# Kernel optimization log

Hardware: AMD Instinct MI355X
Metric: run time of the kernel (lower is better)

Reference implementation:

```python
import jax, jax.numpy as jnp
import numpy as np

B = 8
SHAPE = (4, 16, 16)   # latent video shape; S = prod = 1024
S = 1024
AE = 64               # ae_embed_dim
D = 768               # embed_dim
F = 3072              # mlp_dim
H = 12                # num_heads (heads are re-merged before the score matmul!)
L = 12                # num_layers
C = 17                # n_classes
OUT = 1024            # out_dim
EPS = 1e-6
HD = D // H


def setup_inputs() -> dict:
    key = jax.random.key(0)
    ks = iter(jax.random.split(key, 64))

    def p(shape, s=0.02):
        return jax.random.normal(next(ks), shape, jnp.float32) * s

    inp = {
        'x': jax.random.normal(next(ks), (B, *SHAPE, AE), jnp.float32),
        'mask': jnp.tril(jnp.ones((S, S), bool)),  # causal
        'label': jax.nn.one_hot(jax.random.randint(next(ks), (B,), 0, C), C, dtype=jnp.float32),
        'dense_in_w': p((D, AE)), 'dense_in_b': jnp.zeros((D,), jnp.float32),
        'sos': p((D,)),
        # BroadcastPositionBiases: embed_dim=768 split into 3 chunks of 256
        'pos0': p((SHAPE[0], D // 3)), 'pos1': p((SHAPE[1], D // 3)), 'pos2': p((SHAPE[2], D // 3)),
        'ln1_sw': p((L, D, C)), 'ln1_bw': p((L, D, C)),
        'qkv_w': p((L, 3 * D, D)), 'qkv_b': jnp.zeros((L, 3 * D), jnp.float32),
        'ao1_w': p((L, D, D)), 'ao1_b': jnp.zeros((L, D), jnp.float32),  # DotProductAttention.out_proj
        'ao2_w': p((L, D, D)), 'ao2_b': jnp.zeros((L, D), jnp.float32),  # MultiHeadAttention.out_proj
        'ln2_sw': p((L, D, C)), 'ln2_bw': p((L, D, C)),
        'mlp_w1': p((L, F, D)), 'mlp_b1': jnp.zeros((L, F), jnp.float32),
        'mlp_w2': p((L, D, F)), 'mlp_b2': jnp.zeros((L, D), jnp.float32),
        'lnf_sw': p((D, C)), 'lnf_bw': p((D, C)),
        'out_w': p((OUT, D)), 'out_b': jnp.zeros((OUT,), jnp.float32),
    }
    return inp


def cond_ln(x, cond, sw, bw):
    # conditional LayerNorm: mul = rsqrt(var+eps)*(1+Linear(cond)), bias = Linear(cond)
    mean = jnp.mean(x, axis=-1, keepdims=True)
    var = jnp.mean((x - mean) ** 2, axis=-1, keepdims=True)
    scale = cond @ sw.T   # [B, D]
    bias = cond @ bw.T    # [B, D]
    mul = jax.lax.rsqrt(var + EPS) * (1.0 + scale[:, None, :])
    return (x - mean) * mul + bias[:, None, :]


def pos_bias(embs, shape):
    n = len(shape)
    outs = []
    for i, e in enumerate(embs):
        sh = [1] * n + [e.shape[-1]]
        sh[i] = shape[i]
        outs.append(jnp.broadcast_to(e.reshape(sh), tuple(shape) + (e.shape[-1],)))
    return jnp.concatenate(outs, axis=-1).reshape(-1, sum(e.shape[-1] for e in embs))  # [S, D]


def attn_block(h, mask, qkv_w, qkv_b, o1_w, o1_b, o2_w, o2_b):
    Bn, Sn, Dn = h.shape
    qkv = h @ qkv_w.T + qkv_b                       # [B, S, 3D]
    qkv = qkv.reshape(Bn, Sn, H, 3 * HD)            # per-head [q|k|v] layout
    q = qkv[..., :HD].reshape(Bn, Sn, Dn)           # heads re-merged BEFORE scores
    k = qkv[..., HD:2 * HD].reshape(Bn, Sn, Dn)
    v = qkv[..., 2 * HD:].reshape(Bn, Sn, Dn)
    # NOTE: scaling uses full embed_dim (module quirk), not head_dim
    scores = jnp.einsum('bqd,bkd->bqk', q * (float(Dn) ** -0.5), k)
    scores = jnp.where(mask[None, :, :], scores, -jnp.inf)
    w = jax.nn.softmax(scores, axis=-1)
    out = jnp.einsum('bqk,bkd->bqd', w, v)
    out = out @ o1_w.T + o1_b                        # DotProductAttention.out_proj
    out = out @ o2_w.T + o2_b                        # MultiHeadAttention.out_proj (applied twice)
    return out


def _forward(x, mask, label, dense_in_w, dense_in_b, sos, pos0, pos1, pos2,
             ln1_sw, ln1_bw, qkv_w, qkv_b, ao1_w, ao1_b, ao2_w, ao2_b,
             ln2_sw, ln2_bw, mlp_w1, mlp_b1, mlp_w2, mlp_b2,
             lnf_sw, lnf_bw, out_w, out_b):
    Bn = x.shape[0]
    old_shape = x.shape[1:-1]
    h = x.reshape(Bn, -1, x.shape[-1]) @ dense_in_w.T + dense_in_b   # [B, S, D]
    # right shift with learned SOS token
    h = jnp.concatenate([jnp.broadcast_to(sos, (Bn, 1, D)), h[:, :-1]], axis=1)
    pb = pos_bias([pos0, pos1, pos2], old_shape)                     # [S, D]
    h = h + pb[None, :h.shape[1]]
    for l in range(L):
        hn = cond_ln(h, label, ln1_sw[l], ln1_bw[l])
        h = h + attn_block(hn, mask, qkv_w[l], qkv_b[l], ao1_w[l], ao1_b[l], ao2_w[l], ao2_b[l])
        hn = cond_ln(h, label, ln2_sw[l], ln2_bw[l])
        m = hn @ mlp_w1[l].T + mlp_b1[l]
        m = jax.nn.sigmoid(1.702 * m) * m           # GELU2
        m = m @ mlp_w2[l].T + mlp_b2[l]
        h = h + m
    h = cond_ln(h, label, lnf_sw, lnf_bw)
    out = h @ out_w.T + out_b                        # [B, S, OUT]
    return out.reshape(Bn, *old_shape, out.shape[-1])


def reference(x, mask, label, dense_in_w, dense_in_b, sos, pos0, pos1, pos2,
              ln1_sw, ln1_bw, qkv_w, qkv_b, ao1_w, ao1_b, ao2_w, ao2_b,
              ln2_sw, ln2_bw, mlp_w1, mlp_b1, mlp_w2, mlp_b2,
              lnf_sw, lnf_bw, out_w, out_b):
    return _forward(x, mask, label, dense_in_w, dense_in_b, sos, pos0, pos1, pos2,
                    ln1_sw, ln1_bw, qkv_w, qkv_b, ao1_w, ao1_b, ao2_w, ao2_b,
                    ln2_sw, ln2_bw, mlp_w1, mlp_b1, mlp_w2, mlp_b2,
                    lnf_sw, lnf_bw, out_w, out_b)
```

## Files before the change

### kernel.cpp

```cpp
#include <hip/hip_runtime.h>

typedef __bf16 bf16;
typedef __bf16 bf16x8 __attribute__((ext_vector_type(8)));
typedef __bf16 bf16x4 __attribute__((ext_vector_type(4)));
typedef float  f32x4  __attribute__((ext_vector_type(4)));

#define DEV __device__ __forceinline__

DEV void gload_lds16(const bf16* g, bf16* l) {
    __builtin_amdgcn_global_load_lds(
        (__attribute__((address_space(1))) void*)g,
        (__attribute__((address_space(3))) void*)l, 16, 0, 0);
}

enum { M_QKV, M_SCORES, M_PV, M_BIAS, M_RESID, M_GELU, M_OUT };

template<int MODE>
__global__ __launch_bounds__(256)
void gemm_k(const bf16* __restrict__ A, const bf16* __restrict__ B,
            int M, int N, int K,
            long long batchA, long long batchB, long long batchC,
            const float* __restrict__ bias,
            bf16* __restrict__ Cb, float* __restrict__ Cf,
            bf16* __restrict__ qp, bf16* __restrict__ kp, bf16* __restrict__ vp)
{
    const int bm = blockIdx.x, bn = blockIdx.y, bz = blockIdx.z;
    if (MODE == M_SCORES && bn > bm) return;
    int kTiles = K >> 5;
    if (MODE == M_PV) {
        int lim = (bm + 1) * 4;
        if (lim < kTiles) kTiles = lim;
    }

    const int tid = threadIdx.x, wid = tid >> 6, lane = tid & 63;
    const bf16* Ab = A + (long long)bz * batchA + (long long)bm * 128 * K;
    const bf16* Bb = B + (long long)bz * batchB + (long long)bn * 128 * K;

    __shared__ __align__(16) bf16 sA[2][4096];
    __shared__ __align__(16) bf16 sB[2][4096];

    const int srow = wid * 16 + (lane >> 2);
    const int scol = (lane & 3) * 8;
    const long long aoff = (long long)srow * K + scol;

    auto stage = [&](int buf, int kt) {
        const bf16* ga = Ab + (long long)kt * 32;
        const bf16* gb = Bb + (long long)kt * 32;
        gload_lds16(ga + aoff,            &sA[buf][(wid * 16) * 32]);
        gload_lds16(ga + aoff + 64LL * K, &sA[buf][(64 + wid * 16) * 32]);
        gload_lds16(gb + aoff,            &sB[buf][(wid * 16) * 32]);
        gload_lds16(gb + aoff + 64LL * K, &sB[buf][(64 + wid * 16) * 32]);
    };

    f32x4 acc[4][4];
#pragma unroll
    for (int m = 0; m < 4; ++m)
#pragma unroll
        for (int n = 0; n < 4; ++n) acc[m][n] = (f32x4){0.f, 0.f, 0.f, 0.f};

    stage(0, 0);
    __syncthreads();

    const int wr = wid >> 1, wc = wid & 1;
    const int arow = wr * 64 + (lane & 15);
    const int brow = wc * 64 + (lane & 15);
    const int koff = (lane >> 4) * 8;

    for (int kt = 0; kt < kTiles; ++kt) {
        const int cur = kt & 1;
        if (kt + 1 < kTiles) stage(cur ^ 1, kt + 1);
        bf16x8 af[4], bfr[4];
#pragma unroll
        for (int m = 0; m < 4; ++m)
            af[m] = *(const bf16x8*)&sA[cur][(arow + m * 16) * 32 + koff];
#pragma unroll
        for (int n = 0; n < 4; ++n)
            bfr[n] = *(const bf16x8*)&sB[cur][(brow + n * 16) * 32 + koff];
#pragma unroll
        for (int m = 0; m < 4; ++m)
#pragma unroll
            for (int n = 0; n < 4; ++n)
                acc[m][n] = __builtin_amdgcn_mfma_f32_16x16x32_bf16(af[m], bfr[n], acc[m][n], 0, 0, 0);
        __syncthreads();
    }

    const int cr0 = bm * 128 + wr * 64 + (lane >> 4) * 4;
    const int cc0 = bn * 128 + wc * 64 + (lane & 15);
#pragma unroll
    for (int m = 0; m < 4; ++m) {
#pragma unroll
        for (int n = 0; n < 4; ++n) {
            const int col = cc0 + n * 16;
#pragma unroll
            for (int r = 0; r < 4; ++r) {
                const int row = cr0 + m * 16 + r;
                float v = acc[m][n][r];
                if (MODE == M_QKV) {
                    v += bias[col];
                    int hd = col / 192, rr = col % 192;
                    int b = row >> 10, s = row & 1023;
                    if (rr < 64)
                        qp[(long long)row * 768 + hd * 64 + rr] = (bf16)(v * 0.03608439182435161f);
                    else if (rr < 128)
                        kp[(long long)row * 768 + hd * 64 + (rr - 64)] = (bf16)v;
                    else
                        vp[((long long)b * 768 + hd * 64 + (rr - 128)) * 1024 + s] = (bf16)v;
                } else if (MODE == M_SCORES || MODE == M_PV) {
                    Cb[(long long)bz * batchC + (long long)row * N + col] = (bf16)v;
                } else if (MODE == M_BIAS) {
                    Cb[(long long)row * N + col] = (bf16)(v + bias[col]);
                } else if (MODE == M_RESID) {
                    long long idx = (long long)row * N + col;
                    Cf[idx] += v + bias[col];
                } else if (MODE == M_GELU) {
                    float xg = v + bias[col];
                    Cb[(long long)row * N + col] = (bf16)(xg / (1.f + __expf(-1.702f * xg)));
                } else {
                    Cf[(long long)row * N + col] = v + bias[col];
                }
            }
        }
    }
}

__global__ __launch_bounds__(256)
void cvt_bf16_k(const float* __restrict__ in, bf16* __restrict__ out, int n4)
{
    int i = blockIdx.x * 256 + threadIdx.x;
    if (i >= n4) return;
    float4 f = ((const float4*)in)[i];
    bf16x4 o = { (bf16)f.x, (bf16)f.y, (bf16)f.z, (bf16)f.w };
    ((bf16x4*)out)[i] = o;
}

__global__ __launch_bounds__(256)
void cond_proj_k(const float* __restrict__ label, const float* __restrict__ sw,
                 const float* __restrict__ bw, float* __restrict__ scale,
                 float* __restrict__ bias, int total)
{
    int idx = blockIdx.x * 256 + threadIdx.x;
    if (idx >= total) return;
    int l = idx / 6144;
    int rem = idx - l * 6144;
    int b = rem / 768, d = rem - (rem / 768) * 768;
    const float* lab = label + b * 17;
    const float* swp = sw + ((long long)l * 768 + d) * 17;
    const float* bwp = bw + ((long long)l * 768 + d) * 17;
    float s = 0.f, bb = 0.f;
#pragma unroll
    for (int c = 0; c < 17; ++c) { float lv = lab[c]; s += lv * swp[c]; bb += lv * bwp[c]; }
    scale[idx] = s;
    bias[idx]  = bb;
}

__global__ __launch_bounds__(256)
void embed_k(const float* __restrict__ x, const float* __restrict__ w,
             const float* __restrict__ wb, const float* __restrict__ sos,
             const float* __restrict__ p0, const float* __restrict__ p1,
             const float* __restrict__ p2, float* __restrict__ h)
{
    const int s = blockIdx.x, b = blockIdx.y;
    __shared__ __align__(16) float xr[64];
    if (s > 0 && threadIdx.x < 64)
        xr[threadIdx.x] = x[((long long)b * 1024 + (s - 1)) * 64 + threadIdx.x];
    __syncthreads();
    const int i0 = s >> 8, i1 = (s >> 4) & 15, i2 = s & 15;
#pragma unroll
    for (int j = 0; j < 3; ++j) {
        const int d = j * 256 + threadIdx.x;
        float v;
        if (s == 0) {
            v = sos[d];
        } else {
            const float4* wr4 = (const float4*)(w + (long long)d * 64);
            const float4* xr4 = (const float4*)xr;
            float acc = 0.f;
#pragma unroll
            for (int t = 0; t < 16; ++t) {
                float4 wv = wr4[t], xv = xr4[t];
                acc += wv.x * xv.x + wv.y * xv.y + wv.z * xv.z + wv.w * xv.w;
            }
            v = wb[d] + acc;
        }
        float pbv = (d < 256) ? p0[i0 * 256 + d]
                  : (d < 512) ? p1[i1 * 256 + (d - 256)]
                              : p2[i2 * 256 + (d - 512)];
        h[((long long)b * 1024 + s) * 768 + d] = v + pbv;
    }
}

__global__ __launch_bounds__(256)
void cond_ln_k(const float* __restrict__ h, const float* __restrict__ scale,
               const float* __restrict__ bias, bf16* __restrict__ out)
{
    const long long row = (long long)blockIdx.y * 1024 + blockIdx.x;
    const int b = blockIdx.y;
    const float* hr = h + row * 768;
    float v[3], sum = 0.f, sq = 0.f;
#pragma unroll
    for (int j = 0; j < 3; ++j) {
        v[j] = hr[j * 256 + threadIdx.x];
        sum += v[j]; sq += v[j] * v[j];
    }
    __shared__ float sm[8];
#pragma unroll
    for (int o = 32; o; o >>= 1) { sum += __shfl_down(sum, o); sq += __shfl_down(sq, o); }
    const int wid = threadIdx.x >> 6;
    if ((threadIdx.x & 63) == 0) { sm[wid] = sum; sm[4 + wid] = sq; }
    __syncthreads();
    sum = sm[0] + sm[1] + sm[2] + sm[3];
    sq  = sm[4] + sm[5] + sm[6] + sm[7];
    const float mean = sum * (1.f / 768.f);
    const float var  = sq * (1.f / 768.f) - mean * mean;
    const float rs   = rsqrtf(var + 1e-6f);
    const float* sc = scale + (long long)b * 768;
    const float* bi = bias  + (long long)b * 768;
    bf16* orow = out + row * 768;
#pragma unroll
    for (int j = 0; j < 3; ++j) {
        const int d = j * 256 + threadIdx.x;
        orow[d] = (bf16)((v[j] - mean) * rs * (1.f + sc[d]) + bi[d]);
    }
}

__global__ __launch_bounds__(256)
void softmax_k(bf16* __restrict__ P)
{
    const int i = blockIdx.x, b = blockIdx.y;
    bf16* row = P + ((long long)b * 1024 + i) * 1024;
    const int len = i + 1;
    float v[4], mx = -1e30f;
#pragma unroll
    for (int j = 0; j < 4; ++j) {
        int c = j * 256 + threadIdx.x;
        v[j] = (c < len) ? (float)row[c] : -1e30f;
        mx = fmaxf(mx, v[j]);
    }
    __shared__ float sm[8];
#pragma unroll
    for (int o = 32; o; o >>= 1) mx = fmaxf(mx, __shfl_down(mx, o));
    const int wid = threadIdx.x >> 6;
    if ((threadIdx.x & 63) == 0) sm[wid] = mx;
    __syncthreads();
    mx = fmaxf(fmaxf(sm[0], sm[1]), fmaxf(sm[2], sm[3]));
    float s = 0.f;
#pragma unroll
    for (int j = 0; j < 4; ++j) {
        v[j] = __expf(v[j] - mx);
        s += ((j * 256 + threadIdx.x) < len) ? v[j] : 0.f;
    }
#pragma unroll
    for (int o = 32; o; o >>= 1) s += __shfl_down(s, o);
    if ((threadIdx.x & 63) == 0) sm[4 + wid] = s;
    __syncthreads();
    s = sm[4] + sm[5] + sm[6] + sm[7];
    const float inv = 1.f / s;
#pragma unroll
    for (int j = 0; j < 4; ++j) {
        int c = j * 256 + threadIdx.x;
        row[c] = (c < len) ? (bf16)(v[j] * inv) : (bf16)0.f;
    }
}

__global__ __launch_bounds__(256)
void fill_k(float* o, int n, float v)
{
    int i = blockIdx.x * 256 + threadIdx.x;
    if (i < n) o[i] = v;
}

extern "C" void kernel_launch(void* const* d_in, const int* in_sizes, int n_in,
                              void* d_out, int out_size, void* d_ws, size_t ws_size,
                              hipStream_t stream)
{
    (void)in_sizes; (void)n_in;
    const float* x     = (const float*)d_in[0];
    const float* label = (const float*)d_in[2];
    const float* dw    = (const float*)d_in[3];
    const float* db    = (const float*)d_in[4];
    const float* sos   = (const float*)d_in[5];
    const float* p0    = (const float*)d_in[6];
    const float* p1    = (const float*)d_in[7];
    const float* p2    = (const float*)d_in[8];
    const float* ln1sw = (const float*)d_in[9];
    const float* ln1bw = (const float*)d_in[10];
    const float* qkvw  = (const float*)d_in[11];
    const float* qkvb  = (const float*)d_in[12];
    const float* ao1w  = (const float*)d_in[13];
    const float* ao1b  = (const float*)d_in[14];
    const float* ao2w  = (const float*)d_in[15];
    const float* ao2b  = (const float*)d_in[16];
    const float* ln2sw = (const float*)d_in[17];
    const float* ln2bw = (const float*)d_in[18];
    const float* m1w   = (const float*)d_in[19];
    const float* m1b   = (const float*)d_in[20];
    const float* m2w   = (const float*)d_in[21];
    const float* m2b   = (const float*)d_in[22];
    const float* lnfsw = (const float*)d_in[23];
    const float* lnfbw = (const float*)d_in[24];
    const float* outw  = (const float*)d_in[25];
    const float* outb  = (const float*)d_in[26];
    float* out = (float*)d_out;

    char* p = (char*)d_ws;
    auto alloc = [&](size_t bytes) { void* r = (void*)p; p += (bytes + 255) & ~(size_t)255; return r; };
    float* h    = (float*)alloc(8192LL * 768 * 4);
    bf16*  hn   = (bf16*) alloc(8192LL * 768 * 2);
    bf16*  q    = (bf16*) alloc(8192LL * 768 * 2);
    bf16*  kbuf = (bf16*) alloc(8192LL * 768 * 2);
    bf16*  vT   = (bf16*) alloc(8192LL * 768 * 2);
    bf16*  P    = (bf16*) alloc(8LL * 1024 * 1024 * 2);
    bf16*  attn = (bf16*) alloc(8192LL * 768 * 2);
    bf16*  o1o  = (bf16*) alloc(8192LL * 768 * 2);
    bf16*  mb   = (bf16*) alloc(8192LL * 3072 * 2);
    bf16*  wqkv = (bf16*) alloc(2304LL * 768 * 2);
    bf16*  wo1  = (bf16*) alloc(768LL * 768 * 2);
    bf16*  wo2  = (bf16*) alloc(768LL * 768 * 2);
    bf16*  wm1  = (bf16*) alloc(3072LL * 768 * 2);
    bf16*  wm2  = (bf16*) alloc(3072LL * 768 * 2);
    bf16*  wout = (bf16*) alloc(1024LL * 768 * 2);
    float* s1   = (float*)alloc(12LL * 8 * 768 * 4);
    float* b1   = (float*)alloc(12LL * 8 * 768 * 4);
    float* s2   = (float*)alloc(12LL * 8 * 768 * 4);
    float* b2   = (float*)alloc(12LL * 8 * 768 * 4);
    float* sf   = (float*)alloc(8LL * 768 * 4);
    float* bfb  = (float*)alloc(8LL * 768 * 4);

    size_t needed = (size_t)(p - (char*)d_ws);
    if (needed > ws_size) {
        fill_k<<<(out_size + 255) / 256, 256, 0, stream>>>(out, out_size, 1e9f);
        return;
    }

    cvt_bf16_k<<<1024 * 768 / 4 / 256, 256, 0, stream>>>(outw, wout, 1024 * 768 / 4);
    cond_proj_k<<<(12 * 8 * 768 + 255) / 256, 256, 0, stream>>>(label, ln1sw, ln1bw, s1, b1, 12 * 8 * 768);
    cond_proj_k<<<(12 * 8 * 768 + 255) / 256, 256, 0, stream>>>(label, ln2sw, ln2bw, s2, b2, 12 * 8 * 768);
    cond_proj_k<<<(8 * 768 + 255) / 256, 256, 0, stream>>>(label, lnfsw, lnfbw, sf, bfb, 8 * 768);
    embed_k<<<dim3(1024, 8), 256, 0, stream>>>(x, dw, db, sos, p0, p1, p2, h);

    for (int l = 0; l < 12; ++l) {
        cvt_bf16_k<<<2304 * 768 / 4 / 256, 256, 0, stream>>>(qkvw + (long long)l * 2304 * 768, wqkv, 2304 * 768 / 4);
        cvt_bf16_k<<< 768 * 768 / 4 / 256, 256, 0, stream>>>(ao1w + (long long)l * 768 * 768,  wo1,  768 * 768 / 4);
        cvt_bf16_k<<< 768 * 768 / 4 / 256, 256, 0, stream>>>(ao2w + (long long)l * 768 * 768,  wo2,  768 * 768 / 4);
        cvt_bf16_k<<<3072 * 768 / 4 / 256, 256, 0, stream>>>(m1w  + (long long)l * 3072 * 768, wm1,  3072 * 768 / 4);
        cvt_bf16_k<<<3072 * 768 / 4 / 256, 256, 0, stream>>>(m2w  + (long long)l * 768 * 3072, wm2,  3072 * 768 / 4);

        cond_ln_k<<<dim3(1024, 8), 256, 0, stream>>>(h, s1 + (long long)l * 6144, b1 + (long long)l * 6144, hn);

        gemm_k<M_QKV><<<dim3(64, 18, 1), 256, 0, stream>>>(
            hn, wqkv, 8192, 2304, 768, 0, 0, 0,
            qkvb + (long long)l * 2304, nullptr, nullptr, q, kbuf, vT);

        gemm_k<M_SCORES><<<dim3(8, 8, 8), 256, 0, stream>>>(
            q, kbuf, 1024, 1024, 768, 1024LL * 768, 1024LL * 768, 1024LL * 1024,
            nullptr, P, nullptr, nullptr, nullptr, nullptr);

        softmax_k<<<dim3(1024, 8), 256, 0, stream>>>(P);

        gemm_k<M_PV><<<dim3(8, 6, 8), 256, 0, stream>>>(
            P, vT, 1024, 768, 1024, 1024LL * 1024, 768LL * 1024, 1024LL * 768,
            nullptr, attn, nullptr, nullptr, nullptr, nullptr);

        gemm_k<M_BIAS><<<dim3(64, 6, 1), 256, 0, stream>>>(
            attn, wo1, 8192, 768, 768, 0, 0, 0,
            ao1b + (long long)l * 768, o1o, nullptr, nullptr, nullptr, nullptr);

        gemm_k<M_RESID><<<dim3(64, 6, 1), 256, 0, stream>>>(
            o1o, wo2, 8192, 768, 768, 0, 0, 0,
            ao2b + (long long)l * 768, nullptr, h, nullptr, nullptr, nullptr);

        cond_ln_k<<<dim3(1024, 8), 256, 0, stream>>>(h, s2 + (long long)l * 6144, b2 + (long long)l * 6144, hn);

        gemm_k<M_GELU><<<dim3(64, 24, 1), 256, 0, stream>>>(
            hn, wm1, 8192, 3072, 768, 0, 0, 0,
            m1b + (long long)l * 3072, mb, nullptr, nullptr, nullptr, nullptr);

        gemm_k<M_RESID><<<dim3(64, 6, 1), 256, 0, stream>>>(
            mb, wm2, 8192, 768, 3072, 0, 0, 0,
            m2b + (long long)l * 768, nullptr, h, nullptr, nullptr, nullptr);
    }

    cond_ln_k<<<dim3(1024, 8), 256, 0, stream>>>(h, sf, bfb, hn);
    gemm_k<M_OUT><<<dim3(64, 8, 1), 256, 0, stream>>>(
        hn, wout, 8192, 1024, 768, 0, 0, 0,
        outb, nullptr, out, nullptr, nullptr, nullptr);
}
```

Measured before the change: 4.443 ms.

## Add 256x256-tile 8-wave pipelined GEMM for QKV and MLP1, embed via GEMM

Adds a new GEMM kernel with 512 threads, 256x256 output tiles, a BK=64 double-buffered LDS pipeline loaded through swizzled direct global-to-LDS copies, and MFMA phases interleaved with staging of the next tile. It replaces the generic GEMM for the QKV projection and the first MLP matmul, with the goal of more data reuse per tile and overlap of loads with math. The input embedding is also rewritten as bf16 conversion plus the existing GEMM, followed by a shift-and-position-bias kernel. The large 128KB dynamic LDS limits occupancy to one block per CU, and 288 or 384 blocks over 256 CUs leave an uneven tail wave.

```diff
diff --git a/kernel.cpp b/kernel.cpp
--- a/kernel.cpp
+++ b/kernel.cpp
@@ -11,6 +11,13 @@
     __builtin_amdgcn_global_load_lds(
         (__attribute__((address_space(1))) void*)g,
         (__attribute__((address_space(3))) void*)l, 16, 0, 0);
+}
+
+DEV void memfence_compiler() { asm volatile("" ::: "memory"); }
+DEV void barrier_raw() {
+    memfence_compiler();
+    __builtin_amdgcn_s_barrier();
+    memfence_compiler();
 }
 
 enum { M_QKV, M_SCORES, M_PV, M_BIAS, M_RESID, M_GELU, M_OUT };
@@ -123,6 +130,171 @@
     }
 }
 
+template<int MODE>
+__global__ __launch_bounds__(512, 2)
+void gemm8_k(const bf16* __restrict__ A, const bf16* __restrict__ B,
+             int N, int K, int nbm,
+             const float* __restrict__ bias,
+             bf16* __restrict__ Cb,
+             bf16* __restrict__ qp, bf16* __restrict__ kp, bf16* __restrict__ vp)
+{
+    extern __shared__ __align__(16) bf16 smem[];
+
+    const int cpx = gridDim.x >> 3;
+    const int wgid = (blockIdx.x & 7) * cpx + (blockIdx.x >> 3);
+    const int bm = wgid % nbm, bn = wgid / nbm;
+
+    const int tid = threadIdx.x, w = tid >> 6, l = tid & 63;
+    const bf16* Ab = A + (long long)bm * 256 * K;
+    const bf16* Bb = B + (long long)bn * 256 * K;
+
+    const int sr_base = w * 8 + (l >> 3);
+    const int sg      = ((l & 7) ^ (l >> 3)) << 3;
+    const int dst_off = w * 512;
+
+    auto stage_half = [&](int buf, int kt, int hf) {
+        bf16* aB = smem + buf * 32768 + hf * 8192;
+        bf16* bB = aB + 16384;
+        const bf16* ga = Ab + (long long)(hf * 128) * K + kt * 64 + sg;
+        const bf16* gb = Bb + (long long)(hf * 128) * K + kt * 64 + sg;
+#pragma unroll
+        for (int rd = 0; rd < 2; ++rd) {
+            const long long ro = (long long)(rd * 64 + sr_base) * K;
+            gload_lds16(ga + ro, aB + rd * 4096 + dst_off);
+            gload_lds16(gb + ro, bB + rd * 4096 + dst_off);
+        }
+    };
+
+    const int wr = w >> 2, wc = w & 3;
+    const int l7 = l & 7, l15 = l & 15, lh = l >> 4;
+
+    auto lds_frag = [&](const bf16* base, int row, int s) -> bf16x8 {
+        const int grp = (s * 4 + lh) ^ l7;
+        return *(const bf16x8*)(base + row * 64 + grp * 8);
+    };
+
+    f32x4 acc[8][4];
+#pragma unroll
+    for (int i = 0; i < 8; ++i)
+#pragma unroll
+        for (int j = 0; j < 4; ++j) acc[i][j] = (f32x4){0.f, 0.f, 0.f, 0.f};
+
+    const int nkt = K >> 6;
+
+    stage_half(0, 0, 0); stage_half(0, 0, 1);
+    stage_half(1, 1, 0); stage_half(1, 1, 1);
+    asm volatile("s_waitcnt vmcnt(8)" ::: "memory");
+    barrier_raw();
+
+    bf16x8 a[8][2], b[4][2];
+
+    for (int kt = 0; kt < nkt; ++kt) {
+        const int cur = kt & 1;
+        const bf16* aB = smem + cur * 32768 + (wr * 128) * 64;
+        const bf16* bB = smem + cur * 32768 + 16384 + (wc * 64) * 64;
+
+#pragma unroll
+        for (int i = 0; i < 4; ++i)
+#pragma unroll
+            for (int s = 0; s < 2; ++s) a[i][s] = lds_frag(aB, i * 16 + l15, s);
+#pragma unroll
+        for (int j = 0; j < 2; ++j)
+#pragma unroll
+            for (int s = 0; s < 2; ++s) b[j][s] = lds_frag(bB, j * 16 + l15, s);
+        barrier_raw();
+        __builtin_amdgcn_s_setprio(1);
+#pragma unroll
+        for (int i = 0; i < 4; ++i)
+#pragma unroll
+            for (int j = 0; j < 2; ++j)
+#pragma unroll
+                for (int s = 0; s < 2; ++s)
+                    acc[i][j] = __builtin_amdgcn_mfma_f32_16x16x32_bf16(a[i][s], b[j][s], acc[i][j], 0, 0, 0);
+        __builtin_amdgcn_s_setprio(0);
+        barrier_raw();
+
+#pragma unroll
+        for (int i = 4; i < 8; ++i)
+#pragma unroll
+            for (int s = 0; s < 2; ++s) a[i][s] = lds_frag(aB, i * 16 + l15, s);
+#pragma unroll
+        for (int j = 2; j < 4; ++j)
+#pragma unroll
+            for (int s = 0; s < 2; ++s) b[j][s] = lds_frag(bB, j * 16 + l15, s);
+        barrier_raw();
+        __builtin_amdgcn_s_setprio(1);
+#pragma unroll
+        for (int i = 4; i < 8; ++i)
+#pragma unroll
+            for (int j = 0; j < 2; ++j)
+#pragma unroll
+                for (int s = 0; s < 2; ++s)
+                    acc[i][j] = __builtin_amdgcn_mfma_f32_16x16x32_bf16(a[i][s], b[j][s], acc[i][j], 0, 0, 0);
+        __builtin_amdgcn_s_setprio(0);
+        barrier_raw();
+
+        if (kt + 2 < nkt) stage_half(cur, kt + 2, 0);
+        barrier_raw();
+        __builtin_amdgcn_s_setprio(1);
+#pragma unroll
+        for (int i = 0; i < 4; ++i)
+#pragma unroll
+            for (int j = 2; j < 4; ++j)
+#pragma unroll
+                for (int s = 0; s < 2; ++s)
+                    acc[i][j] = __builtin_amdgcn_mfma_f32_16x16x32_bf16(a[i][s], b[j][s], acc[i][j], 0, 0, 0);
+        __builtin_amdgcn_s_setprio(0);
+        barrier_raw();
+
+        if (kt + 2 < nkt) stage_half(cur, kt + 2, 1);
+        barrier_raw();
+        __builtin_amdgcn_s_setprio(1);
+#pragma unroll
+        for (int i = 4; i < 8; ++i)
+#pragma unroll
+            for (int j = 2; j < 4; ++j)
+#pragma unroll
+                for (int s = 0; s < 2; ++s)
+                    acc[i][j] = __builtin_amdgcn_mfma_f32_16x16x32_bf16(a[i][s], b[j][s], acc[i][j], 0, 0, 0);
+        __builtin_amdgcn_s_setprio(0);
+
+        if (kt + 1 < nkt) {
+            if (kt + 2 < nkt) asm volatile("s_waitcnt vmcnt(8)" ::: "memory");
+            else              asm volatile("s_waitcnt vmcnt(0)" ::: "memory");
+            barrier_raw();
+        }
+    }
+
+    const int row0 = bm * 256 + wr * 128 + lh * 4;
+    const int col0 = bn * 256 + wc * 64 + l15;
+#pragma unroll
+    for (int i = 0; i < 8; ++i) {
+#pragma unroll
+        for (int j = 0; j < 4; ++j) {
+            const int col = col0 + j * 16;
+#pragma unroll
+            for (int r = 0; r < 4; ++r) {
+                const int row = row0 + i * 16 + r;
+                float v = acc[i][j][r];
+                if (MODE == M_QKV) {
+                    v += bias[col];
+                    int hd = col / 192, rr = col % 192;
+                    int bb = row >> 10, s = row & 1023;
+                    if (rr < 64)
+                        qp[(long long)row * 768 + hd * 64 + rr] = (bf16)(v * 0.03608439182435161f);
+                    else if (rr < 128)
+                        kp[(long long)row * 768 + hd * 64 + (rr - 64)] = (bf16)v;
+                    else
+                        vp[((long long)bb * 768 + hd * 64 + (rr - 128)) * 1024 + s] = (bf16)v;
+                } else {
+                    float xg = v + bias[col];
+                    Cb[(long long)row * N + col] = (bf16)(xg / (1.f + __expf(-1.702f * xg)));
+                }
+            }
+        }
+    }
+}
+
 __global__ __launch_bounds__(256)
 void cvt_bf16_k(const float* __restrict__ in, bf16* __restrict__ out, int n4)
 {
@@ -154,34 +326,17 @@
 }
 
 __global__ __launch_bounds__(256)
-void embed_k(const float* __restrict__ x, const float* __restrict__ w,
-             const float* __restrict__ wb, const float* __restrict__ sos,
-             const float* __restrict__ p0, const float* __restrict__ p1,
-             const float* __restrict__ p2, float* __restrict__ h)
+void shift_pos_k(const float* __restrict__ xe, const float* __restrict__ sos,
+                 const float* __restrict__ p0, const float* __restrict__ p1,
+                 const float* __restrict__ p2, float* __restrict__ h)
 {
     const int s = blockIdx.x, b = blockIdx.y;
-    __shared__ __align__(16) float xr[64];
-    if (s > 0 && threadIdx.x < 64)
-        xr[threadIdx.x] = x[((long long)b * 1024 + (s - 1)) * 64 + threadIdx.x];
-    __syncthreads();
     const int i0 = s >> 8, i1 = (s >> 4) & 15, i2 = s & 15;
+    const float* xr = xe + ((long long)b * 1024 + (s - 1)) * 768;
 #pragma unroll
     for (int j = 0; j < 3; ++j) {
         const int d = j * 256 + threadIdx.x;
-        float v;
-        if (s == 0) {
-            v = sos[d];
-        } else {
-            const float4* wr4 = (const float4*)(w + (long long)d * 64);
-            const float4* xr4 = (const float4*)xr;
-            float acc = 0.f;
-#pragma unroll
-            for (int t = 0; t < 16; ++t) {
-                float4 wv = wr4[t], xv = xr4[t];
-                acc += wv.x * xv.x + wv.y * xv.y + wv.z * xv.z + wv.w * xv.w;
-            }
-            v = wb[d] + acc;
-        }
+        float v = (s == 0) ? sos[d] : xr[d];
         float pbv = (d < 256) ? p0[i0 * 256 + d]
                   : (d < 512) ? p1[i1 * 256 + (d - 256)]
                               : p2[i2 * 256 + (d - 512)];
@@ -326,6 +481,10 @@
     float* sf   = (float*)alloc(8LL * 768 * 4);
     float* bfb  = (float*)alloc(8LL * 768 * 4);
 
+    bf16*  xbf  = (bf16*)P;
+    bf16*  dwbf = (bf16*)(P + 1024 * 1024);
+    float* xe   = (float*)mb;
+
     size_t needed = (size_t)(p - (char*)d_ws);
     if (needed > ws_size) {
         fill_k<<<(out_size + 255) / 256, 256, 0, stream>>>(out, out_size, 1e9f);
@@ -336,7 +495,12 @@
     cond_proj_k<<<(12 * 8 * 768 + 255) / 256, 256, 0, stream>>>(label, ln1sw, ln1bw, s1, b1, 12 * 8 * 768);
     cond_proj_k<<<(12 * 8 * 768 + 255) / 256, 256, 0, stream>>>(label, ln2sw, ln2bw, s2, b2, 12 * 8 * 768);
     cond_proj_k<<<(8 * 768 + 255) / 256, 256, 0, stream>>>(label, lnfsw, lnfbw, sf, bfb, 8 * 768);
-    embed_k<<<dim3(1024, 8), 256, 0, stream>>>(x, dw, db, sos, p0, p1, p2, h);
+
+    cvt_bf16_k<<<8192 * 64 / 4 / 256, 256, 0, stream>>>(x, xbf, 8192 * 64 / 4);
+    cvt_bf16_k<<<768 * 64 / 4 / 256, 256, 0, stream>>>(dw, dwbf, 768 * 64 / 4);
+    gemm_k<M_OUT><<<dim3(64, 6, 1), 256, 0, stream>>>(
+        xbf, dwbf, 8192, 768, 64, 0, 0, 0, db, nullptr, xe, nullptr, nullptr, nullptr);
+    shift_pos_k<<<dim3(1024, 8), 256, 0, stream>>>(xe, sos, p0, p1, p2, h);
 
     for (int l = 0; l < 12; ++l) {
         cvt_bf16_k<<<2304 * 768 / 4 / 256, 256, 0, stream>>>(qkvw + (long long)l * 2304 * 768, wqkv, 2304 * 768 / 4);
@@ -347,9 +511,9 @@
 
         cond_ln_k<<<dim3(1024, 8), 256, 0, stream>>>(h, s1 + (long long)l * 6144, b1 + (long long)l * 6144, hn);
 
-        gemm_k<M_QKV><<<dim3(64, 18, 1), 256, 0, stream>>>(
-            hn, wqkv, 8192, 2304, 768, 0, 0, 0,
-            qkvb + (long long)l * 2304, nullptr, nullptr, q, kbuf, vT);
+        gemm8_k<M_QKV><<<288, 512, 131072, stream>>>(
+            hn, wqkv, 2304, 768, 32,
+            qkvb + (long long)l * 2304, nullptr, q, kbuf, vT);
 
         gemm_k<M_SCORES><<<dim3(8, 8, 8), 256, 0, stream>>>(
             q, kbuf, 1024, 1024, 768, 1024LL * 768, 1024LL * 768, 1024LL * 1024,
@@ -371,9 +535,9 @@
 
         cond_ln_k<<<dim3(1024, 8), 256, 0, stream>>>(h, s2 + (long long)l * 6144, b2 + (long long)l * 6144, hn);
 
-        gemm_k<M_GELU><<<dim3(64, 24, 1), 256, 0, stream>>>(
-            hn, wm1, 8192, 3072, 768, 0, 0, 0,
-            m1b + (long long)l * 3072, mb, nullptr, nullptr, nullptr, nullptr);
+        gemm8_k<M_GELU><<<384, 512, 131072, stream>>>(
+            hn, wm1, 3072, 768, 32,
+            m1b + (long long)l * 3072, mb, nullptr, nullptr, nullptr);
 
         gemm_k<M_RESID><<<dim3(64, 6, 1), 256, 0, stream>>>(
             mb, wm2, 8192, 768, 3072, 0, 0, 0,
```

Measured after the change: 4.556 ms. 2.5% more time.
